# Kernel optimization log

Measured on AMD Instinct MI355X. Metric: run time of the kernel, lower is better.

Reference implementation:

```python
import jax, jax.numpy as jnp
import numpy as np

B, T, C = 4, 2048, 1024
H = 16
DH = C // H
DFF = 4 * C


def _layernorm(x, g, b, eps=1e-5):
    mu = jnp.mean(x, axis=-1, keepdims=True)
    var = jnp.var(x, axis=-1, keepdims=True)
    return (x - mu) * jax.lax.rsqrt(var + eps) * g + b


def setup_inputs() -> dict:
    key = jax.random.key(0)
    ks = jax.random.split(key, 12)
    s = 0.02
    return {
        "x": jax.random.normal(ks[0], (B, T, C), jnp.float32),
        "Wq": jax.random.normal(ks[1], (H, C, DH), jnp.float32) * s,
        "bq": jnp.zeros((H, DH), jnp.float32),
        "Wk": jax.random.normal(ks[2], (H, C, DH), jnp.float32) * s,
        "bk": jnp.zeros((H, DH), jnp.float32),
        "Wv": jax.random.normal(ks[3], (H, C, DH), jnp.float32) * s,
        "bv": jnp.zeros((H, DH), jnp.float32),
        "Wo": jax.random.normal(ks[4], (C, C), jnp.float32) * s,
        "bo": jnp.zeros((C,), jnp.float32),
        "ln1_g": jnp.ones((C,), jnp.float32),
        "ln1_b": jnp.zeros((C,), jnp.float32),
        "ln2_g": jnp.ones((C,), jnp.float32),
        "ln2_b": jnp.zeros((C,), jnp.float32),
        "W1": jax.random.normal(ks[5], (C, DFF), jnp.float32) * s,
        "b1": jnp.zeros((DFF,), jnp.float32),
        "W2": jax.random.normal(ks[6], (DFF, C), jnp.float32) * s,
        "b2": jnp.zeros((C,), jnp.float32),
    }


def reference(x, Wq, bq, Wk, bk, Wv, bv, Wo, bo, ln1_g, ln1_b, ln2_g, ln2_b, W1, b1, W2, b2):
    # pre-norm for attention
    xn = _layernorm(x, ln1_g, ln1_b)
    # per-head projections, batched: [B,H,T,DH]
    q = jnp.einsum("btc,hcd->bhtd", xn, Wq) + bq[None, :, None, :]
    k = jnp.einsum("btc,hcd->bhtd", xn, Wk) + bk[None, :, None, :]
    v = jnp.einsum("btc,hcd->bhtd", xn, Wv) + bv[None, :, None, :]
    # FAITHFUL to source: scores / scale with scale = DH**-0.5, i.e. * sqrt(DH)
    scores = jnp.einsum("bhtd,bhsd->bhts", q, k) * jnp.sqrt(jnp.float32(DH))
    attn = jax.nn.softmax(scores, axis=-1)
    o = jnp.einsum("bhts,bhsd->bhtd", attn, v)  # [B,H,T,DH]
    # concat heads along last dim (head order matches ModuleList concat)
    o = jnp.transpose(o, (0, 2, 1, 3)).reshape(B, T, C)
    attn_out = o @ Wo + bo  # dropout is identity at eval
    x = x + attn_out
    xn2 = _layernorm(x, ln2_g, ln2_b)
    ffn = jax.nn.relu(xn2 @ W1 + b1) @ W2 + b2
    return x + ffn
```

## Files before the change

kernel.cpp:

```cpp
#include <hip/hip_runtime.h>
#include <hip/hip_bf16.h>
#include <stdint.h>

typedef unsigned short ushort_t;
typedef short short8 __attribute__((ext_vector_type(8)));
typedef unsigned short ushortx8 __attribute__((ext_vector_type(8)));
typedef float floatx4 __attribute__((ext_vector_type(4)));

template <int N> struct IC { static constexpr int value = N; };
template <bool B> struct BC { static constexpr bool value = B; };

#define SBAR() asm volatile("s_barrier" ::: "memory")

__device__ __forceinline__ float b2f(ushort_t u) {
    return __uint_as_float(((unsigned int)u) << 16);
}
__device__ __forceinline__ ushort_t f2bf(float f) {
    unsigned int u = __float_as_uint(f);
    unsigned int r = u + 0x7FFFu + ((u >> 16) & 1u);
    return (ushort_t)(r >> 16);
}
__device__ __forceinline__ unsigned int cvtpk(float lo, float hi) {
    unsigned int r;
    asm("v_cvt_pk_bf16_f32 %0, %1, %2" : "=v"(r) : "v"(lo), "v"(hi));
    return r;
}
__device__ __forceinline__ void gll16(const void* g, void* l) {
    __builtin_amdgcn_global_load_lds((const __attribute__((address_space(1))) unsigned int*)g,
                                     (__attribute__((address_space(3))) unsigned int*)l,
                                     16, 0, 0);
}

__global__ void transpose_kernel(const float* __restrict__ in, ushort_t* __restrict__ out,
                                 int K, int N) {
    __shared__ float tile[32][33];
    in += (long)blockIdx.z * K * N;
    out += (long)blockIdx.z * K * N;
    int k0 = blockIdx.x * 32, n0 = blockIdx.y * 32;
    int x = threadIdx.x, y = threadIdx.y;
#pragma unroll
    for (int i = 0; i < 4; i++)
        tile[y + 8 * i][x] = in[(long)(k0 + y + 8 * i) * N + n0 + x];
    __syncthreads();
#pragma unroll
    for (int i = 0; i < 4; i++)
        out[(long)(n0 + y + 8 * i) * K + k0 + x] = f2bf(tile[x][y + 8 * i]);
}

__global__ void concat_bias_kernel(const float* __restrict__ bq, const float* __restrict__ bk,
                                   const float* __restrict__ bv, float* __restrict__ dst) {
    int i = blockIdx.x * 256 + threadIdx.x;
    dst[i] = i < 1024 ? bq[i] : (i < 2048 ? bk[i - 1024] : bv[i - 2048]);
}

__global__ __launch_bounds__(256) void ln_kernel(const float* __restrict__ in,
                                                 ushort_t* __restrict__ out,
                                                 const float* __restrict__ g,
                                                 const float* __restrict__ b) {
    long row = blockIdx.x;
    int tid = threadIdx.x;
    float4 v4 = *((const float4*)(in + row * 1024) + tid);
    float v[4] = {v4.x, v4.y, v4.z, v4.w};
    float s1 = v[0] + v[1] + v[2] + v[3];
    float s2 = v[0] * v[0] + v[1] * v[1] + v[2] * v[2] + v[3] * v[3];
#pragma unroll
    for (int m = 32; m >= 1; m >>= 1) {
        s1 += __shfl_xor(s1, m);
        s2 += __shfl_xor(s2, m);
    }
    __shared__ float r1[4], r2[4];
    int w = tid >> 6;
    if ((tid & 63) == 0) { r1[w] = s1; r2[w] = s2; }
    __syncthreads();
    s1 = r1[0] + r1[1] + r1[2] + r1[3];
    s2 = r2[0] + r2[1] + r2[2] + r2[3];
    float mu = s1 * (1.0f / 1024.0f);
    float var = s2 * (1.0f / 1024.0f) - mu * mu;
    float inv = rsqrtf(var + 1e-5f);
    float y[4];
#pragma unroll
    for (int i = 0; i < 4; i++)
        y[i] = (v[i] - mu) * inv * g[tid * 4 + i] + b[tid * 4 + i];
    unsigned int lo = (unsigned int)f2bf(y[0]) | ((unsigned int)f2bf(y[1]) << 16);
    unsigned int hi = (unsigned int)f2bf(y[2]) | ((unsigned int)f2bf(y[3]) << 16);
    *(uint2*)(out + row * 1024 + tid * 4) = make_uint2(lo, hi);
}

template <typename OutT, int RELU, int MODE>
__device__ __forceinline__ void gemm128(
    const ushort_t* __restrict__ A, int lda,
    const ushort_t* __restrict__ Bt, int ldb, int K,
    OutT* __restrict__ C, long cBatch, int ldc,
    const float* __restrict__ bias, const float* __restrict__ resid,
    ushort_t* As, ushort_t* Bs) {
    int m0 = blockIdx.x * 128, n0 = blockIdx.y * 128;
    int tid = threadIdx.x, lane = tid & 63, w = tid >> 6;
    int ln = lane & 15, quad = lane >> 4;
    int wr = w >> 1, wc = w & 1;
    int lr = lane >> 2, lc = (lane & 3) * 8;

    auto stage = [&](int k0, int buf) {
#pragma unroll
        for (int i = 0; i < 4; i++) {
            int id = w * 4 + i;
            int blk = id & 7;
            int row = blk * 16 + lr;
            if (id < 8)
                gll16(A + (long)(m0 + row) * lda + k0 + lc, As + buf * 4096 + blk * 512);
            else
                gll16(Bt + (long)(n0 + row) * ldb + k0 + lc, Bs + buf * 4096 + blk * 512);
        }
    };

    floatx4 acc[4][4];
#pragma unroll
    for (int a = 0; a < 4; a++)
#pragma unroll
        for (int bb = 0; bb < 4; bb++) acc[a][bb] = floatx4{0, 0, 0, 0};

    stage(0, 0);
    int cur = 0;
    for (int k0 = 0; k0 < K; k0 += 32, cur ^= 1) {
        __syncthreads();
        if (k0 + 32 < K) stage(k0 + 32, cur ^ 1);
        const ushort_t* Ab = As + cur * 4096;
        const ushort_t* Bb = Bs + cur * 4096;
        short8 af[4], bf[4];
#pragma unroll
        for (int j = 0; j < 4; j++) {
            af[j] = *(const short8*)(Ab + (wr * 64 + j * 16 + ln) * 32 + quad * 8);
            bf[j] = *(const short8*)(Bb + (wc * 64 + j * 16 + ln) * 32 + quad * 8);
        }
#pragma unroll
        for (int a = 0; a < 4; a++)
#pragma unroll
            for (int bb = 0; bb < 4; bb++)
                acc[a][bb] = __builtin_amdgcn_mfma_f32_16x16x32_bf16(af[a], bf[bb], acc[a][bb], 0, 0, 0);
    }
#pragma unroll
    for (int bb = 0; bb < 4; bb++) {
        int gn = n0 + wc * 64 + bb * 16 + ln;
        float bv = bias ? bias[gn] : 0.0f;
#pragma unroll
        for (int a = 0; a < 4; a++) {
#pragma unroll
            for (int r = 0; r < 4; r++) {
                int gm = m0 + wr * 64 + a * 16 + quad * 4 + r;
                float val = acc[a][bb][r] + bv;
                if (RELU) val = fmaxf(val, 0.0f);
                long off = (long)(gm >> 11) * cBatch + (long)(gm & 2047) * ldc + gn;
                if (resid) val += resid[off];
                if constexpr (sizeof(OutT) == 2)
                    C[off] = (OutT)f2bf(val);
                else
                    C[off] = (OutT)val;
            }
        }
    }
}

__global__ __launch_bounds__(256) void gemm128_f32_kernel(
    const ushort_t* __restrict__ A, int lda, const ushort_t* __restrict__ Bt, int ldb, int K,
    float* __restrict__ C, long cBatch, int ldc,
    const float* __restrict__ bias, const float* __restrict__ resid) {
    __shared__ ushort_t As[2 * 128 * 32];
    __shared__ ushort_t Bs[2 * 128 * 32];
    gemm128<float, 0, 0>(A, lda, Bt, ldb, K, C, cBatch, ldc, bias, resid, As, Bs);
}

template <int RELU, int MODE>
__device__ __forceinline__ void gemm256(
    const ushort_t* __restrict__ A, int lda,
    const ushort_t* __restrict__ Bt, int ldb, int K, int ntn,
    ushort_t* __restrict__ C, long cBatch, int ldc,
    const float* __restrict__ bias, ushort_t* lds) {
    int nwg = gridDim.x;
    int wg = ((int)blockIdx.x & 7) * (nwg >> 3) + ((int)blockIdx.x >> 3);
    int m0 = (wg / ntn) * 256, n0 = (wg % ntn) * 256;
    int tid = threadIdx.x, lane = tid & 63, w = tid >> 6;
    int ln = lane & 15, quad = lane >> 4;
    int wm = w >> 2, wn = w & 3;
    int lr = lane >> 2, lq = lane & 3;
    int ssw = (lr >> 1) & 3, rsw = (ln >> 1) & 3;

    const ushort_t* pa[2];
    const ushort_t* pb[2];
#pragma unroll
    for (int i = 0; i < 2; i++) {
        int id = w * 2 + i;
        pa[i] = A + (long)(m0 + id * 16 + lr) * lda + ((lq ^ ssw) << 3);
        pb[i] = Bt + (long)(n0 + id * 16 + lr) * ldb + ((lq ^ ssw) << 3);
    }
    auto stageA = [&](int t) {
        ushort_t* d = lds + (t & 3) * 16384;
#pragma unroll
        for (int i = 0; i < 2; i++) gll16(pa[i] + t * 32, d + (w * 2 + i) * 512);
    };
    auto stageB = [&](int t) {
        ushort_t* d = lds + (t & 3) * 16384 + 8192;
#pragma unroll
        for (int i = 0; i < 2; i++) gll16(pb[i] + t * 32, d + (w * 2 + i) * 512);
    };

    floatx4 acc[8][4];
#pragma unroll
    for (int a = 0; a < 8; a++)
#pragma unroll
        for (int bb = 0; bb < 4; bb++) acc[a][bb] = floatx4{0, 0, 0, 0};

    stageA(0); stageB(0); stageA(1); stageB(1); stageA(2); stageB(2);
    asm volatile("s_waitcnt vmcnt(8)" ::: "memory");
    SBAR();

    int NT = K >> 5;
    auto iter = [&](int t, auto vmc, auto stc) {
        constexpr int VM = decltype(vmc)::value;
        constexpr bool ST = decltype(stc)::value;
        const ushort_t* Ab = lds + (t & 3) * 16384;
        const ushort_t* Bb = Ab + 8192;
        short8 af[4], bf[4];
#pragma unroll
        for (int j = 0; j < 4; j++)
            bf[j] = *(const short8*)(Bb + (wn * 64 + j * 16 + ln) * 32 + ((quad ^ rsw) << 3));
#pragma unroll
        for (int j = 0; j < 4; j++)
            af[j] = *(const short8*)(Ab + (wm * 128 + j * 16 + ln) * 32 + ((quad ^ rsw) << 3));
        if constexpr (ST) stageA(t + 3);
        SBAR();
        __builtin_amdgcn_s_setprio(1);
#pragma unroll
        for (int a = 0; a < 4; a++)
#pragma unroll
            for (int bb = 0; bb < 4; bb++)
                acc[a][bb] = __builtin_amdgcn_mfma_f32_16x16x32_bf16(af[a], bf[bb], acc[a][bb], 0, 0, 0);
        __builtin_amdgcn_s_setprio(0);
        SBAR();
#pragma unroll
        for (int j = 0; j < 4; j++)
            af[j] = *(const short8*)(Ab + (wm * 128 + 64 + j * 16 + ln) * 32 + ((quad ^ rsw) << 3));
        if constexpr (ST) stageB(t + 3);
        SBAR();
        __builtin_amdgcn_s_setprio(1);
#pragma unroll
        for (int a = 0; a < 4; a++)
#pragma unroll
            for (int bb = 0; bb < 4; bb++)
                acc[a + 4][bb] = __builtin_amdgcn_mfma_f32_16x16x32_bf16(af[a], bf[bb], acc[a + 4][bb], 0, 0, 0);
        __builtin_amdgcn_s_setprio(0);
        if constexpr (VM == 8)
            asm volatile("s_waitcnt vmcnt(8)" ::: "memory");
        else if constexpr (VM == 4)
            asm volatile("s_waitcnt vmcnt(4)" ::: "memory");
        else
            asm volatile("s_waitcnt vmcnt(0)" ::: "memory");
        SBAR();
    };

    for (int t = 0; t < NT - 3; ++t) iter(t, IC<8>{}, BC<true>{});
    iter(NT - 3, IC<4>{}, BC<false>{});
    iter(NT - 2, IC<0>{}, BC<false>{});
    iter(NT - 1, IC<0>{}, BC<false>{});

#pragma unroll
    for (int bb = 0; bb < 4; bb++) {
        int gn = n0 + wn * 64 + bb * 16 + ln;
        float bv = bias[gn];
#pragma unroll
        for (int a = 0; a < 8; a++) {
#pragma unroll
            for (int r = 0; r < 4; r++) {
                int gm = m0 + wm * 128 + a * 16 + quad * 4 + r;
                float val = acc[a][bb][r] + bv;
                if (RELU) val = fmaxf(val, 0.0f);
                long off;
                if constexpr (MODE == 2) {
                    int gnl = gn & 1023;
                    if (gn < 2048)
                        off = (long)(gn >> 10) * 8388608 + (long)(gm >> 11) * 2097152 +
                              (long)(gm & 2047) * 1024 + gnl;
                    else
                        off = 16777216L +
                              ((((long)(gm >> 11)) * 16 + (gnl >> 6)) * 64 + (gnl & 63)) * 2048 +
                              (gm & 2047);
                } else {
                    off = (long)(gm >> 11) * cBatch + (long)(gm & 2047) * ldc + gn;
                }
                C[off] = f2bf(val);
            }
        }
    }
}

__global__ __launch_bounds__(512, 2) void gemm256_qkv_kernel(
    const ushort_t* __restrict__ A, const ushort_t* __restrict__ Bt,
    ushort_t* __restrict__ C, const float* __restrict__ bias) {
    __shared__ ushort_t lds[4 * 16384];
    gemm256<0, 2>(A, 1024, Bt, 1024, 1024, 12, C, 0, 0, bias, lds);
}

__global__ __launch_bounds__(512, 2) void gemm256_relu_kernel(
    const ushort_t* __restrict__ A, const ushort_t* __restrict__ Bt,
    ushort_t* __restrict__ C, const float* __restrict__ bias) {
    __shared__ ushort_t lds[4 * 16384];
    gemm256<1, 0>(A, 1024, Bt, 1024, 1024, 8, C, 2048L * 2048, 2048, bias, lds);
}

__global__ __launch_bounds__(512, 4) void attn_kernel(
    const ushort_t* __restrict__ q, const ushort_t* __restrict__ k,
    const ushort_t* __restrict__ vt, ushort_t* __restrict__ o) {
    __shared__ ushort_t Klds[2 * 4096];
    __shared__ ushort_t Vlds[2 * 4096];
    int flat = blockIdx.x;
    int bh = (flat & 7) * 8 + (flat >> 6);
    int xt = (flat >> 3) & 7;
    int b = bh >> 4, h = bh & 15;
    int t0 = xt * 256;
    int tid = threadIdx.x, lane = tid & 63, w = tid >> 6;
    int ln = lane & 15, quad = lane >> 4;
    int lr = lane >> 2, lq = lane & 3;
    int bsrc = (lane & 48) + ((lane >> 4) << 2);
    int rsw = (ln >> 1) & 3;
    int ssw = (lr >> 1) & 3;

    const ushort_t* qbase = q + ((long)b * 2048 + t0 + w * 32) * 1024 + h * 64;
    short8 qf[2][2];
#pragma unroll
    for (int sub = 0; sub < 2; sub++)
#pragma unroll
        for (int s = 0; s < 2; s++) {
            ushortx8 t = *(const ushortx8*)(qbase + (long)(sub * 16 + ln) * 1024 + s * 32 + quad * 8);
#pragma unroll
            for (int j = 0; j < 8; j++) qf[sub][s][j] = (short)f2bf(b2f(t[j]) * 8.0f);
        }

    floatx4 O[2][4];
    float m_i[2] = {-1e30f, -1e30f}, l_i[2] = {0.0f, 0.0f};
#pragma unroll
    for (int sub = 0; sub < 2; sub++)
#pragma unroll
        for (int i = 0; i < 4; i++) O[sub][i] = floatx4{0, 0, 0, 0};

    long krow0 = (long)b * 2048 * 1024 + h * 64;
    const ushort_t* vbase = vt + (long)bh * 64 * 2048;

    auto stage = [&](int kv0, int buf) {
#pragma unroll
        for (int i = 0; i < 2; i++) {
            int id = w * 2 + i;
            int s = (id >> 2) & 1, qt = id & 3;
            int cs = ((lq ^ ssw) << 3);
            if (id < 8) {
                int prow = ((qt >> 1) << 5) + ((lr >> 2) << 3) + ((qt & 1) << 2) + (lr & 3);
                gll16(k + krow0 + (long)(kv0 + prow) * 1024 + s * 32 + cs,
                      Klds + buf * 4096 + s * 2048 + qt * 512);
            } else {
                int row = qt * 16 + lr;
                gll16(vbase + (long)row * 2048 + kv0 + s * 32 + cs,
                      Vlds + buf * 4096 + s * 2048 + qt * 512);
            }
        }
    };

    stage(0, 0);
    int cur = 0;
    for (int t32 = 0; t32 < 32; t32++, cur ^= 1) {
        __syncthreads();
        if (t32 < 31) stage((t32 + 1) * 64, cur ^ 1);
        const ushort_t* Kb = Klds + cur * 4096;
        const ushort_t* Vb = Vlds + cur * 4096;

        floatx4 Z[2][4];
#pragma unroll
        for (int sub = 0; sub < 2; sub++)
#pragma unroll
            for (int nc = 0; nc < 4; nc++) Z[sub][nc] = floatx4{0, 0, 0, 0};
#pragma unroll
        for (int s = 0; s < 2; s++)
#pragma unroll
            for (int nc = 0; nc < 4; nc++) {
                short8 kf = *(const short8*)(Kb + s * 2048 + (nc * 16 + ln) * 32 + ((quad ^ rsw) << 3));
                Z[0][nc] = __builtin_amdgcn_mfma_f32_16x16x32_bf16(kf, qf[0][s], Z[0][nc], 0, 0, 0);
                Z[1][nc] = __builtin_amdgcn_mfma_f32_16x16x32_bf16(kf, qf[1][s], Z[1][nc], 0, 0, 0);
            }

        float alpha[2];
        short8 pf[2][2];
#pragma unroll
        for (int sub = 0; sub < 2; sub++) {
            float mx = -1e30f;
#pragma unroll
            for (int nc = 0; nc < 4; nc++)
#pragma unroll
                for (int r = 0; r < 4; r++) mx = fmaxf(mx, Z[sub][nc][r]);
            mx = fmaxf(mx, __shfl_xor(mx, 16));
            mx = fmaxf(mx, __shfl_xor(mx, 32));
            float nm = fmaxf(m_i[sub], mx);
            alpha[sub] = __expf(m_i[sub] - nm);
            m_i[sub] = nm;
            float rs = 0.0f;
#pragma unroll
            for (int s = 0; s < 2; s++) {
                float a0 = __expf(Z[sub][2 * s][0] - nm), a1 = __expf(Z[sub][2 * s][1] - nm);
                float a2 = __expf(Z[sub][2 * s][2] - nm), a3 = __expf(Z[sub][2 * s][3] - nm);
                float b0 = __expf(Z[sub][2 * s + 1][0] - nm), b1 = __expf(Z[sub][2 * s + 1][1] - nm);
                float b2 = __expf(Z[sub][2 * s + 1][2] - nm), b3 = __expf(Z[sub][2 * s + 1][3] - nm);
                rs += ((a0 + a1) + (a2 + a3)) + ((b0 + b1) + (b2 + b3));
                union { unsigned int u[4]; short8 v; } pu;
                pu.u[0] = cvtpk(a0, a1);
                pu.u[1] = cvtpk(a2, a3);
                pu.u[2] = cvtpk(b0, b1);
                pu.u[3] = cvtpk(b2, b3);
                pf[sub][s] = pu.v;
            }
            rs += __shfl_xor(rs, 16);
            rs += __shfl_xor(rs, 32);
            l_i[sub] = l_i[sub] * alpha[sub] + rs;
        }
#pragma unroll
        for (int sub = 0; sub < 2; sub++)
#pragma unroll
            for (int r = 0; r < 4; r++) {
                float ar = __shfl(alpha[sub], bsrc + r);
#pragma unroll
                for (int dc = 0; dc < 4; dc++) O[sub][dc][r] *= ar;
            }
#pragma unroll
        for (int s = 0; s < 2; s++)
#pragma unroll
            for (int dc = 0; dc < 4; dc++) {
                short8 vf = *(const short8*)(Vb + s * 2048 + (dc * 16 + ln) * 32 + ((quad ^ rsw) << 3));
                O[0][dc] = __builtin_amdgcn_mfma_f32_16x16x32_bf16(pf[0][s], vf, O[0][dc], 0, 0, 0);
                O[1][dc] = __builtin_amdgcn_mfma_f32_16x16x32_bf16(pf[1][s], vf, O[1][dc], 0, 0, 0);
            }
    }
#pragma unroll
    for (int sub = 0; sub < 2; sub++)
#pragma unroll
        for (int r = 0; r < 4; r++) {
            float inv = 1.0f / __shfl(l_i[sub], bsrc + r);
            int t = t0 + w * 32 + sub * 16 + quad * 4 + r;
            ushort_t* orow = o + ((long)b * 2048 + t) * 1024 + h * 64;
#pragma unroll
            for (int dc = 0; dc < 4; dc++) orow[dc * 16 + ln] = f2bf(O[sub][dc][r] * inv);
        }
}

extern "C" void kernel_launch(void* const* d_in, const int* in_sizes, int n_in,
                              void* d_out, int out_size, void* d_ws, size_t ws_size,
                              hipStream_t stream) {
    const float* x   = (const float*)d_in[0];
    const float* Wq  = (const float*)d_in[1];
    const float* bq  = (const float*)d_in[2];
    const float* Wk  = (const float*)d_in[3];
    const float* bk  = (const float*)d_in[4];
    const float* Wv  = (const float*)d_in[5];
    const float* bv  = (const float*)d_in[6];
    const float* Wo  = (const float*)d_in[7];
    const float* bo  = (const float*)d_in[8];
    const float* g1  = (const float*)d_in[9];
    const float* be1 = (const float*)d_in[10];
    const float* g2  = (const float*)d_in[11];
    const float* be2 = (const float*)d_in[12];
    const float* W1  = (const float*)d_in[13];
    const float* b1  = (const float*)d_in[14];
    const float* W2  = (const float*)d_in[15];
    const float* b2  = (const float*)d_in[16];
    float* out = (float*)d_out;

    const long MB = 1 << 20;
    char* w = (char*)d_ws;
    ushort_t* xn  = (ushort_t*)(w);
    float*    x2  = (float*)(w + 16 * MB);
    ushort_t* qb  = (ushort_t*)(w + 48 * MB);
    ushort_t* kb  = (ushort_t*)(w + 64 * MB);
    ushort_t* vtb = (ushort_t*)(w + 80 * MB);
    ushort_t* xn2 = qb;
    ushort_t* h1  = (ushort_t*)(w + 64 * MB);
    ushort_t* WqT = (ushort_t*)(w + 96 * MB);
    ushort_t* WkT = (ushort_t*)(w + 98 * MB);
    ushort_t* WvT = (ushort_t*)(w + 100 * MB);
    ushort_t* WoT = (ushort_t*)(w + 102 * MB);
    ushort_t* W1T = (ushort_t*)(w + 104 * MB);
    ushort_t* W2T = (ushort_t*)(w + 112 * MB);
    float* biasCat = x2;

    dim3 tb(32, 8);
    transpose_kernel<<<dim3(32, 2, 16), tb, 0, stream>>>(Wq, WqT, 1024, 64);
    transpose_kernel<<<dim3(32, 2, 16), tb, 0, stream>>>(Wk, WkT, 1024, 64);
    transpose_kernel<<<dim3(32, 2, 16), tb, 0, stream>>>(Wv, WvT, 1024, 64);
    transpose_kernel<<<dim3(32, 32, 1), tb, 0, stream>>>(Wo, WoT, 1024, 1024);
    transpose_kernel<<<dim3(32, 128, 1), tb, 0, stream>>>(W1, W1T, 1024, 4096);
    transpose_kernel<<<dim3(128, 32, 1), tb, 0, stream>>>(W2, W2T, 4096, 1024);
    concat_bias_kernel<<<12, 256, 0, stream>>>(bq, bk, bv, biasCat);

    ln_kernel<<<8192, 256, 0, stream>>>(x, xn, g1, be1);
    gemm256_qkv_kernel<<<384, 512, 0, stream>>>(xn, WqT, qb, biasCat);
    attn_kernel<<<512, 512, 0, stream>>>(qb, kb, vtb, xn );
    gemm128_f32_kernel<<<dim3(64, 8), 256, 0, stream>>>(xn, 1024, WoT, 1024, 1024,
                                                        x2, 2048L * 1024, 1024, bo, x);
    ln_kernel<<<8192, 256, 0, stream>>>((const float*)x2, xn2, g2, be2);
    gemm256_relu_kernel<<<256, 512, 0, stream>>>(xn2, W1T, h1, b1);
    gemm128_f32_kernel<<<dim3(64, 8), 256, 0, stream>>>(
        h1, 2048, W2T, 4096, 2048, out, 2048L * 1024, 1024, b2, x2);
    gemm256_relu_kernel<<<256, 512, 0, stream>>>(xn2, W1T + 2048L * 1024, h1, b1 + 2048);
    gemm128_f32_kernel<<<dim3(64, 8), 256, 0, stream>>>(
        h1, 2048, W2T + 2048, 4096, 2048, out, 2048L * 1024, 1024, nullptr, out);
}
```

Before: 580.0 us.

## Restructure 256-tile GEMM to K=64 steps with double-buffered LDS

Replaces the 4-stage K=32 pipeline with split A/B staging and interleaved barriers by a 2-stage pipeline over K=64 tiles, using an 8-way XOR swizzle and loading all 8 A fragments per k-substep. This halves the number of loop iterations and barriers and issues larger MFMA batches between syncs. The cost is shallower prefetch, since only one tile is in flight and each iteration waits on vmcnt(0). Register pressure also rises from holding 8 A fragments at once.

```diff
diff --git a/kernel.cpp b/kernel.cpp
--- a/kernel.cpp
+++ b/kernel.cpp
@@ -6,9 +6,6 @@
 typedef short short8 __attribute__((ext_vector_type(8)));
 typedef unsigned short ushortx8 __attribute__((ext_vector_type(8)));
 typedef float floatx4 __attribute__((ext_vector_type(4)));
-
-template <int N> struct IC { static constexpr int value = N; };
-template <bool B> struct BC { static constexpr bool value = B; };
 
 #define SBAR() asm volatile("s_barrier" ::: "memory")
 
@@ -86,7 +83,7 @@
     *(uint2*)(out + row * 1024 + tid * 4) = make_uint2(lo, hi);
 }
 
-template <typename OutT, int RELU, int MODE>
+template <typename OutT, int RELU>
 __device__ __forceinline__ void gemm128(
     const ushort_t* __restrict__ A, int lda,
     const ushort_t* __restrict__ Bt, int ldb, int K,
@@ -165,11 +162,11 @@
     const float* __restrict__ bias, const float* __restrict__ resid) {
     __shared__ ushort_t As[2 * 128 * 32];
     __shared__ ushort_t Bs[2 * 128 * 32];
-    gemm128<float, 0, 0>(A, lda, Bt, ldb, K, C, cBatch, ldc, bias, resid, As, Bs);
+    gemm128<float, 0>(A, lda, Bt, ldb, K, C, cBatch, ldc, bias, resid, As, Bs);
 }
 
 template <int RELU, int MODE>
-__device__ __forceinline__ void gemm256(
+__device__ __forceinline__ void gemm256k64(
     const ushort_t* __restrict__ A, int lda,
     const ushort_t* __restrict__ Bt, int ldb, int K, int ntn,
     ushort_t* __restrict__ C, long cBatch, int ldc,
@@ -180,86 +177,63 @@
     int tid = threadIdx.x, lane = tid & 63, w = tid >> 6;
     int ln = lane & 15, quad = lane >> 4;
     int wm = w >> 2, wn = w & 3;
-    int lr = lane >> 2, lq = lane & 3;
-    int ssw = (lr >> 1) & 3, rsw = (ln >> 1) & 3;
-
-    const ushort_t* pa[2];
-    const ushort_t* pb[2];
-#pragma unroll
-    for (int i = 0; i < 2; i++) {
-        int id = w * 2 + i;
-        pa[i] = A + (long)(m0 + id * 16 + lr) * lda + ((lq ^ ssw) << 3);
-        pb[i] = Bt + (long)(n0 + id * 16 + lr) * ldb + ((lq ^ ssw) << 3);
-    }
-    auto stageA = [&](int t) {
-        ushort_t* d = lds + (t & 3) * 16384;
-#pragma unroll
-        for (int i = 0; i < 2; i++) gll16(pa[i] + t * 32, d + (w * 2 + i) * 512);
+    int rsw8 = (ln >> 1) & 7;
+    int srow = w * 8 + (lane >> 3);
+    int sswz = (w * 4 + (lane >> 4)) & 7;
+    int scol = ((lane & 7) ^ sswz) * 8;
+
+    const ushort_t* pa[4];
+    const ushort_t* pb[4];
+#pragma unroll
+    for (int r = 0; r < 4; r++) {
+        pa[r] = A + (long)(m0 + r * 64 + srow) * lda + scol;
+        pb[r] = Bt + (long)(n0 + r * 64 + srow) * ldb + scol;
+    }
+    auto stage = [&](int t) {
+        ushort_t* dst = lds + (t & 1) * 32768;
+        int wb = w * 512;
+#pragma unroll
+        for (int r = 0; r < 4; r++) gll16(pa[r] + t * 64, dst + r * 4096 + wb);
+#pragma unroll
+        for (int r = 0; r < 4; r++) gll16(pb[r] + t * 64, dst + 16384 + r * 4096 + wb);
     };
-    auto stageB = [&](int t) {
-        ushort_t* d = lds + (t & 3) * 16384 + 8192;
-#pragma unroll
-        for (int i = 0; i < 2; i++) gll16(pb[i] + t * 32, d + (w * 2 + i) * 512);
-    };
 
     floatx4 acc[8][4];
 #pragma unroll
-    for (int a = 0; a < 8; a++)
-#pragma unroll
-        for (int bb = 0; bb < 4; bb++) acc[a][bb] = floatx4{0, 0, 0, 0};
-
-    stageA(0); stageB(0); stageA(1); stageB(1); stageA(2); stageB(2);
-    asm volatile("s_waitcnt vmcnt(8)" ::: "memory");
+    for (int m = 0; m < 8; m++)
+#pragma unroll
+        for (int n = 0; n < 4; n++) acc[m][n] = floatx4{0, 0, 0, 0};
+
+    int NT = K >> 6;
+    stage(0);
+    asm volatile("s_waitcnt vmcnt(0)" ::: "memory");
     SBAR();
 
-    int NT = K >> 5;
-    auto iter = [&](int t, auto vmc, auto stc) {
-        constexpr int VM = decltype(vmc)::value;
-        constexpr bool ST = decltype(stc)::value;
-        const ushort_t* Ab = lds + (t & 3) * 16384;
-        const ushort_t* Bb = Ab + 8192;
-        short8 af[4], bf[4];
-#pragma unroll
-        for (int j = 0; j < 4; j++)
-            bf[j] = *(const short8*)(Bb + (wn * 64 + j * 16 + ln) * 32 + ((quad ^ rsw) << 3));
-#pragma unroll
-        for (int j = 0; j < 4; j++)
-            af[j] = *(const short8*)(Ab + (wm * 128 + j * 16 + ln) * 32 + ((quad ^ rsw) << 3));
-        if constexpr (ST) stageA(t + 3);
+    for (int t = 0; t < NT; ++t) {
+        if (t + 1 < NT) stage(t + 1);
+        const ushort_t* Ab = lds + (t & 1) * 32768;
+        const ushort_t* Bb = Ab + 16384;
+#pragma unroll
+        for (int ks = 0; ks < 2; ks++) {
+            short8 af[8], bf[4];
+            int sl = (((ks << 2) | quad) ^ rsw8) << 3;
+#pragma unroll
+            for (int m = 0; m < 8; m++)
+                af[m] = *(const short8*)(Ab + (wm * 128 + m * 16 + ln) * 64 + sl);
+#pragma unroll
+            for (int n = 0; n < 4; n++)
+                bf[n] = *(const short8*)(Bb + (wn * 64 + n * 16 + ln) * 64 + sl);
+            __builtin_amdgcn_s_setprio(1);
+#pragma unroll
+            for (int m = 0; m < 8; m++)
+#pragma unroll
+                for (int n = 0; n < 4; n++)
+                    acc[m][n] = __builtin_amdgcn_mfma_f32_16x16x32_bf16(af[m], bf[n], acc[m][n], 0, 0, 0);
+            __builtin_amdgcn_s_setprio(0);
+        }
+        asm volatile("s_waitcnt vmcnt(0)" ::: "memory");
         SBAR();
-        __builtin_amdgcn_s_setprio(1);
-#pragma unroll
-        for (int a = 0; a < 4; a++)
-#pragma unroll
-            for (int bb = 0; bb < 4; bb++)
-                acc[a][bb] = __builtin_amdgcn_mfma_f32_16x16x32_bf16(af[a], bf[bb], acc[a][bb], 0, 0, 0);
-        __builtin_amdgcn_s_setprio(0);
-        SBAR();
-#pragma unroll
-        for (int j = 0; j < 4; j++)
-            af[j] = *(const short8*)(Ab + (wm * 128 + 64 + j * 16 + ln) * 32 + ((quad ^ rsw) << 3));
-        if constexpr (ST) stageB(t + 3);
-        SBAR();
-        __builtin_amdgcn_s_setprio(1);
-#pragma unroll
-        for (int a = 0; a < 4; a++)
-#pragma unroll
-            for (int bb = 0; bb < 4; bb++)
-                acc[a + 4][bb] = __builtin_amdgcn_mfma_f32_16x16x32_bf16(af[a], bf[bb], acc[a + 4][bb], 0, 0, 0);
-        __builtin_amdgcn_s_setprio(0);
-        if constexpr (VM == 8)
-            asm volatile("s_waitcnt vmcnt(8)" ::: "memory");
-        else if constexpr (VM == 4)
-            asm volatile("s_waitcnt vmcnt(4)" ::: "memory");
-        else
-            asm volatile("s_waitcnt vmcnt(0)" ::: "memory");
-        SBAR();
-    };
-
-    for (int t = 0; t < NT - 3; ++t) iter(t, IC<8>{}, BC<true>{});
-    iter(NT - 3, IC<4>{}, BC<false>{});
-    iter(NT - 2, IC<0>{}, BC<false>{});
-    iter(NT - 1, IC<0>{}, BC<false>{});
+    }
 
 #pragma unroll
     for (int bb = 0; bb < 4; bb++) {
@@ -294,15 +268,15 @@
 __global__ __launch_bounds__(512, 2) void gemm256_qkv_kernel(
     const ushort_t* __restrict__ A, const ushort_t* __restrict__ Bt,
     ushort_t* __restrict__ C, const float* __restrict__ bias) {
-    __shared__ ushort_t lds[4 * 16384];
-    gemm256<0, 2>(A, 1024, Bt, 1024, 1024, 12, C, 0, 0, bias, lds);
+    __shared__ ushort_t lds[2 * 32768];
+    gemm256k64<0, 2>(A, 1024, Bt, 1024, 1024, 12, C, 0, 0, bias, lds);
 }
 
 __global__ __launch_bounds__(512, 2) void gemm256_relu_kernel(
     const ushort_t* __restrict__ A, const ushort_t* __restrict__ Bt,
     ushort_t* __restrict__ C, const float* __restrict__ bias) {
-    __shared__ ushort_t lds[4 * 16384];
-    gemm256<1, 0>(A, 1024, Bt, 1024, 1024, 8, C, 2048L * 2048, 2048, bias, lds);
+    __shared__ ushort_t lds[2 * 32768];
+    gemm256k64<1, 0>(A, 1024, Bt, 1024, 1024, 8, C, 2048L * 2048, 2048, bias, lds);
 }
 
 __global__ __launch_bounds__(512, 4) void attn_kernel(
```

New measurement: 569.6 us. About the same (-1.8%).
